# Optimization experiments

Measured on AMD Instinct MI355X. Metric: run time of the kernel, lower is better.

## Reference

```python
import jax, jax.numpy as jnp
import numpy as np
from jax import lax

V_PATCH_NUMS = (1, 2, 4, 8, 16)
BETA = 0.25
QUANT_RESI = 0.5
NUM_PHI = 4  # share_quant_resi=4 -> PhiPartiallyShared

# PhiPartiallyShared tick lookup (K=4 -> linspace(1/12, 11/12, 4))
def _phi_indices():
    K = NUM_PHI
    ticks = np.linspace(1/3/K, 1 - 1/3/K, K) if K == 4 else np.linspace(1/2/K, 1 - 1/2/K, K)
    SN = len(V_PATCH_NUMS)
    return [int(np.argmin(np.abs(ticks - si/(SN-1)))) for si in range(SN)]

PHI_IDX = _phi_indices()  # [0, 1, 1, 2, 3]


def phi_apply(h, w, b, ratio=QUANT_RESI):
    # h_out = (1-a)*h + a*Conv3x3(h), padding=1
    conv = lax.conv_general_dilated(h, w, (1, 1), 'SAME',
                                    dimension_numbers=('NCHW', 'OIHW', 'NCHW'))
    conv = conv + b[None, :, None, None]
    return h * (1.0 - ratio) + conv * ratio


def vq_forward(f_BChw, emb_w, phi_w, phi_b):
    f = f_BChw.astype(jnp.float32)
    B, C, H, W = f.shape
    f_ng = lax.stop_gradient(f)
    f_rest = f_ng
    f_hat = jnp.zeros_like(f)
    SN = len(V_PATCH_NUMS)
    loss = jnp.float32(0.0)
    emb_ng = lax.stop_gradient(emb_w)  # distances use .data (no grad)
    e_sq = jnp.sum(emb_ng * emb_ng, axis=1)  # [V]
    for si, pn in enumerate(V_PATCH_NUMS):
        if si != SN - 1:
            k = H // pn  # exact area pooling (divisible sizes)
            z = f_rest.reshape(B, C, pn, k, pn, k).mean(axis=(3, 5))
        else:
            z = f_rest
        z_NC = z.transpose(0, 2, 3, 1).reshape(-1, C)  # [B*pn*pn, C]
        # squared L2 distance to every code, argmin
        d = (jnp.sum(z_NC * z_NC, axis=1, keepdims=True) + e_sq
             - 2.0 * z_NC @ emb_ng.T)  # [N, V]
        idx = jnp.argmin(d, axis=1)  # [N]
        h = emb_w[idx].reshape(B, pn, pn, C).transpose(0, 3, 1, 2)  # [B,C,pn,pn]
        if si != SN - 1:
            h = jax.image.resize(h, (B, C, H, W), method='cubic')  # bicubic upsample
        pi = PHI_IDX[si]
        h = phi_apply(h, phi_w[pi], phi_b[pi])
        f_hat = f_hat + h
        f_rest = f_rest - h
        loss = loss + (BETA * jnp.mean((lax.stop_gradient(f_hat) - f) ** 2)
                       + jnp.mean((f_hat - f_ng) ** 2))
    loss = loss / SN
    # straight-through estimator
    f_hat_out = lax.stop_gradient(f_hat) - f_ng + f
    return f_hat_out, loss


def setup_inputs() -> dict:
    key = jax.random.key(0)
    k1, k2, k3 = jax.random.split(key, 3)
    B, C, H, W = 64, 32, 16, 16
    V = 4096
    f_BChw = jax.random.normal(k1, (B, C, H, W), dtype=jnp.float32)
    emb_w = jax.random.normal(k2, (V, C), dtype=jnp.float32) * 0.5
    phi_w = jax.random.normal(k3, (NUM_PHI, C, C, 3, 3), dtype=jnp.float32) * 0.05
    phi_b = jnp.zeros((NUM_PHI, C), dtype=jnp.float32)
    return {'f_BChw': f_BChw, 'emb_w': emb_w, 'phi_w': phi_w, 'phi_b': phi_b}


def reference(f_BChw, emb_w, phi_w, phi_b):
    return vq_forward(f_BChw, emb_w, phi_w, phi_b)
```

## Files before the change

### kernel.cpp

```cpp
#include <hip/hip_runtime.h>

typedef unsigned long long u64;

#define B_ 64
#define C_ 32
#define H_ 16
#define W_ 16
#define V_ 4096
#define NELEM_ (B_*C_*H_*W_)
#define NPOS_TOTAL 21824


__device__ __forceinline__ float keys_cubic(float x) {
  if (x >= 2.f) return 0.f;
  if (x >= 1.f) return ((-0.5f*x + 2.5f)*x - 4.f)*x + 2.f;
  return (1.5f*x - 2.5f)*x*x + 1.f;
}

__device__ __forceinline__ u64 pack_key(float d, int idx) {
  unsigned bu = __float_as_uint(d);
  unsigned m = bu ^ ((bu >> 31) ? 0xFFFFFFFFu : 0x80000000u);
  return ((u64)m << 32) | (unsigned)idx;
}


__global__ void init_kernel(const float* __restrict__ f, const float* __restrict__ emb,
                            float* __restrict__ f_rest, float* __restrict__ f_hat,
                            float* __restrict__ e_sq, u64* __restrict__ part,
                            float* __restrict__ loss_part) {
  int i = blockIdx.x*blockDim.x + threadIdx.x;
  if (i < NELEM_) { f_rest[i] = f[i]; f_hat[i] = 0.f; }
  if (i < NPOS_TOTAL) part[i] = ~0ull;
  if (i < 5*256) loss_part[i] = 0.f;
  if (i < V_) {
    const float4* p = (const float4*)(emb + (size_t)i*32);
    float s = 0.f;
#pragma unroll
    for (int j = 0; j < 8; ++j) { float4 q = p[j]; s += q.x*q.x + q.y*q.y + q.z*q.z + q.w*q.w; }
    e_sq[i] = s;
  }
}


__global__ void pool_kernel(const float* __restrict__ f_rest, float* __restrict__ z,
                            int pn, int k) {
  int t = blockIdx.x*blockDim.x + threadIdx.x;
  int N = B_*pn*pn;
  if (t >= N*C_) return;
  int n = t >> 5, c = t & 31;
  int pn2 = pn*pn;
  int b = n / pn2, rem = n % pn2;
  int y = rem / pn, x = rem % pn;
  const float* base = f_rest + (((size_t)b*C_ + c)*H_ + y*k)*W_ + x*k;
  float s = 0.f;
  if (k >= 4) {
    const float4* b4 = (const float4*)base;
    for (int ky = 0; ky < k; ++ky)
      for (int kx = 0; kx < (k>>2); ++kx) {
        float4 q = b4[ky*4 + kx];
        s += (q.x + q.y) + (q.z + q.w);
      }
  } else if (k == 2) {
    const float2* b2 = (const float2*)base;
    s = (b2[0].x + b2[0].y) + (b2[8].x + b2[8].y);
  } else {
    s = base[0];
  }
  z[(size_t)n*32 + c] = s * (1.f/(float)(k*k));
}


template<int P, int TILE>
__global__ void __launch_bounds__(256) argmin2_kernel(
    const float* __restrict__ z, const float* __restrict__ emb,
    const float* __restrict__ e_sq, u64* __restrict__ part, int cpc) {
  __shared__ float cl[TILE*32];
  __shared__ float es[TILE];
  const int tid = threadIdx.x;
  const int n0 = blockIdx.x*256*P + tid;
  float zb[P][32]; float zz[P];
#pragma unroll
  for (int p = 0; p < P; ++p) {
    const float4* zp = (const float4*)(z + (size_t)(n0 + p*256)*32);
#pragma unroll
    for (int i = 0; i < 8; ++i) {
      float4 q = zp[i];
      zb[p][4*i+0]=q.x; zb[p][4*i+1]=q.y; zb[p][4*i+2]=q.z; zb[p][4*i+3]=q.w;
    }
    float s = 0.f;
#pragma unroll
    for (int i = 0; i < 32; ++i) s = fmaf(zb[p][i], zb[p][i], s);
    zz[p] = s;
  }
  const int v0 = blockIdx.y * cpc;
  float bd[P]; int bi[P];
#pragma unroll
  for (int p = 0; p < P; ++p) { bd[p] = 3.4e38f; bi[p] = 0; }
  for (int t0 = 0; t0 < cpc; t0 += TILE) {
    __syncthreads();
    const float4* src = (const float4*)(emb + (size_t)(v0 + t0)*32);
    for (int e = tid; e < TILE*8; e += 256) ((float4*)cl)[e] = src[e];
    if (tid < TILE) es[tid] = e_sq[v0 + t0 + tid];
    __syncthreads();
    for (int c = 0; c < TILE; ++c) {
      const float4* cp = (const float4*)(cl + c*32);
      float4 q[8];
#pragma unroll
      for (int i = 0; i < 8; ++i) q[i] = cp[i];
      float ev = es[c];
#pragma unroll
      for (int p = 0; p < P; ++p) {
        float a0=0.f, a1=0.f, a2=0.f, a3=0.f;
#pragma unroll
        for (int i = 0; i < 8; ++i) {
          a0 = fmaf(zb[p][4*i+0], q[i].x, a0);
          a1 = fmaf(zb[p][4*i+1], q[i].y, a1);
          a2 = fmaf(zb[p][4*i+2], q[i].z, a2);
          a3 = fmaf(zb[p][4*i+3], q[i].w, a3);
        }
        float dot = (a0+a1)+(a2+a3);
        float d = (zz[p] + ev) - 2.f*dot;
        bool lt = d < bd[p];
        bd[p] = lt ? d : bd[p];
        bi[p] = lt ? (v0 + t0 + c) : bi[p];
      }
    }
  }
#pragma unroll
  for (int p = 0; p < P; ++p)
    atomicMin(part + n0 + p*256, pack_key(bd[p], bi[p]));
}

__global__ void __launch_bounds__(256) argmin0_kernel(
    const float* __restrict__ z, const float* __restrict__ emb,
    const float* __restrict__ e_sq, u64* __restrict__ part) {
  __shared__ float cl[64*32];
  __shared__ float es[64];
  const int tid = threadIdx.x;
  const int v0 = blockIdx.x * 64;
  const float4* src = (const float4*)(emb + (size_t)v0*32);
  for (int e = tid; e < 64*8; e += 256) ((float4*)cl)[e] = src[e];
  if (tid < 64) es[tid] = e_sq[v0 + tid];
  __syncthreads();
  const int p = tid & 63, sub = tid >> 6;
  float zb[32];
  const float4* zp = (const float4*)(z + (size_t)p*32);
#pragma unroll
  for (int i = 0; i < 8; ++i) {
    float4 q = zp[i];
    zb[4*i+0]=q.x; zb[4*i+1]=q.y; zb[4*i+2]=q.z; zb[4*i+3]=q.w;
  }
  float zz = 0.f;
#pragma unroll
  for (int i = 0; i < 32; ++i) zz = fmaf(zb[i], zb[i], zz);
  float bd = 3.4e38f; int bi = 0;
  for (int c = sub*16; c < sub*16 + 16; ++c) {
    const float4* cp = (const float4*)(cl + c*32);
    float4 q[8];
#pragma unroll
    for (int i = 0; i < 8; ++i) q[i] = cp[i];
    float a0=0.f, a1=0.f, a2=0.f, a3=0.f;
#pragma unroll
    for (int i = 0; i < 8; ++i) {
      a0 = fmaf(zb[4*i+0], q[i].x, a0);
      a1 = fmaf(zb[4*i+1], q[i].y, a1);
      a2 = fmaf(zb[4*i+2], q[i].z, a2);
      a3 = fmaf(zb[4*i+3], q[i].w, a3);
    }
    float dot = (a0+a1)+(a2+a3);
    float d = (zz + es[c]) - 2.f*dot;
    if (d < bd) { bd = d; bi = v0 + c; }
  }
  atomicMin(part + p, pack_key(bd, bi));
}


template<int PN>
__global__ void __launch_bounds__(512) upconv_kernel(
    const u64* __restrict__ part_s,
    const float* __restrict__ emb,
    const float* __restrict__ phi_w,
    const float* __restrict__ phi_b,
    const float* __restrict__ f,
    float* __restrict__ f_hat,
    float* __restrict__ f_rest,
    float* __restrict__ loss_part)
{
  constexpr int PN2 = PN*PN;
  const int b = blockIdx.x;
  const int cg = blockIdx.y;
  const int tid = threadIdx.x;

  __shared__ int   idx_s[PN2];
  __shared__ float W4[16][4];
  __shared__ int   I0[16];
  __shared__ float tmp_s[(PN < 16) ? C_*PN*16 : 1];
  union HupHs { float hup[C_*16*18]; float hs[C_*16*18]; };
  __shared__ HupHs u;
  __shared__ float wsum[8];

  for (int p = tid; p < PN2; p += 512)
    idx_s[p] = (int)(part_s[b*PN2 + p] & 0xFFFFFFFFull);

  if (PN < 16 && tid < 16) {
    float sf = (tid + 0.5f) * ((float)PN/16.f) - 0.5f;
    int i0 = (int)floorf(sf) - 1;
    float w[4]; float tot = 0.f;
#pragma unroll
    for (int t = 0; t < 4; ++t) {
      int i = i0 + t;
      float wv = (i >= 0 && i < PN) ? keys_cubic(fabsf(sf - (float)i)) : 0.f;
      w[t] = wv; tot += wv;
    }
    float r = 1.f/tot;
#pragma unroll
    for (int t = 0; t < 4; ++t) W4[tid][t] = w[t]*r;
    I0[tid] = i0;
  }
  __syncthreads();

  if (PN < 16) {
    for (int e = tid; e < C_*PN2; e += 512) {
      int c = e / PN2, p = e % PN2;
      u.hs[c*PN2 + p] = emb[(size_t)idx_s[p]*32 + c];
    }
  } else {
    for (int e = tid; e < C_*256; e += 512) {
      int c = e >> 8, p = e & 255;
      int y = p >> 4, x = p & 15;
      u.hup[(c*16 + y)*18 + 1 + x] = emb[(size_t)idx_s[p]*32 + c];
    }
    for (int e = tid; e < C_*16; e += 512) { u.hup[e*18] = 0.f; u.hup[e*18 + 17] = 0.f; }
  }
  __syncthreads();

  if (PN < 16) {
    for (int e = tid; e < C_*PN*16; e += 512) {
      int jx = e & 15; int rest = e >> 4;
      int iy = rest % PN; int c = rest / PN;
      int i0 = I0[jx];
      float s = 0.f;
#pragma unroll
      for (int t = 0; t < 4; ++t) {
        int ix = i0 + t; int ixc = min(max(ix, 0), PN-1);
        s += W4[jx][t] * u.hs[(c*PN + iy)*PN + ixc];
      }
      tmp_s[(c*PN + iy)*16 + jx] = s;
    }
    __syncthreads();
    for (int e = tid; e < C_*16; e += 512) { u.hup[e*18] = 0.f; u.hup[e*18 + 17] = 0.f; }
    for (int e = tid; e < C_*256; e += 512) {
      int jx = e & 15; int jy = (e >> 4) & 15; int c = e >> 8;
      int i0 = I0[jy];
      float s = 0.f;
#pragma unroll
      for (int t = 0; t < 4; ++t) {
        int iy = i0 + t; int iyc = min(max(iy, 0), PN-1);
        s += W4[jy][t] * tmp_s[(c*PN + iyc)*16 + jx];
      }
      u.hup[(c*16 + jy)*18 + 1 + jx] = s;
    }
    __syncthreads();
  }

  const int px = tid & 255;
  const int g  = tid >> 8;
  const int y  = px >> 4, x = px & 15;
  const int co0 = cg*8 + g*4;
  const float* wbase = phi_w + (size_t)co0*32*9;
  float acc[4];
#pragma unroll
  for (int o = 0; o < 4; ++o) acc[o] = phi_b[co0 + o];
  for (int ci = 0; ci < 32; ++ci) {
    float wn[9];
#pragma unroll
    for (int ky = 0; ky < 3; ++ky) {
      int yy = y + ky - 1;
      bool v = (yy >= 0 && yy <= 15);
      const float* r = &u.hup[(ci*16 + (v ? yy : 0))*18 + x];
      wn[ky*3+0] = v ? r[0] : 0.f;
      wn[ky*3+1] = v ? r[1] : 0.f;
      wn[ky*3+2] = v ? r[2] : 0.f;
    }
#pragma unroll
    for (int o = 0; o < 4; ++o) {
      const float* wp = wbase + ((size_t)o*32 + ci)*9;
#pragma unroll
      for (int t = 0; t < 9; ++t) acc[o] = fmaf(wp[t], wn[t], acc[o]);
    }
  }
  float lsum = 0.f;
#pragma unroll
  for (int o = 0; o < 4; ++o) {
    int co = co0 + o;
    float hv = 0.5f*u.hup[(co*16 + y)*18 + 1 + x] + 0.5f*acc[o];
    size_t gi = (((size_t)b*C_ + co)*16 + y)*16 + x;
    float fh = f_hat[gi] + hv;
    f_hat[gi] = fh;
    f_rest[gi] -= hv;
    float dd = fh - f[gi];
    lsum = fmaf(dd, dd, lsum);
  }
#pragma unroll
  for (int off = 32; off > 0; off >>= 1) lsum += __shfl_down(lsum, off);
  if ((tid & 63) == 0) wsum[tid >> 6] = lsum;
  __syncthreads();
  if (tid == 0) {
    float s = 0.f;
#pragma unroll
    for (int i = 0; i < 8; ++i) s += wsum[i];
    loss_part[blockIdx.y*64 + blockIdx.x] = s;
  }
}

__global__ void loss_kernel(const float* __restrict__ loss_part, float* __restrict__ out_loss) {
  __shared__ float s[256];
  int t = threadIdx.x;
  float v = 0.f;
#pragma unroll
  for (int i = 0; i < 5; ++i) v += loss_part[i*256 + t];
  s[t] = v;
  __syncthreads();
  for (int off = 128; off > 0; off >>= 1) {
    if (t < off) s[t] += s[t + off];
    __syncthreads();
  }
  if (t == 0) out_loss[0] = s[0] * (1.25f / (5.f * (float)NELEM_));
}


extern "C" void kernel_launch(void* const* d_in, const int* in_sizes, int n_in,
                              void* d_out, int out_size, void* d_ws, size_t ws_size,
                              hipStream_t stream) {
  const float* f     = (const float*)d_in[0];
  const float* emb   = (const float*)d_in[1];
  const float* phi_w = (const float*)d_in[2];
  const float* phi_b = (const float*)d_in[3];
  float* f_hat    = (float*)d_out;
  float* out_loss = f_hat + NELEM_;

  char* ws = (char*)d_ws;
  float* f_rest = (float*)ws;
  float* z      = f_rest + NELEM_;
  u64*   part   = (u64*)(z + NELEM_);
  float* e_sq   = (float*)(part + NPOS_TOTAL);
  float* loss_part = e_sq + V_;

  init_kernel<<<NELEM_/256, 256, 0, stream>>>(f, emb, f_rest, f_hat, e_sq, part, loss_part);

  const int PNs[5]   = {1,2,4,8,16};
  const int PHI[5]   = {0,1,2,2,3};
  const int PBASE[5] = {0, 64, 320, 1344, 5440};

  for (int si = 0; si < 5; ++si) {
    int pn = PNs[si], k = 16/pn, N = B_*pn*pn;
    pool_kernel<<<(N*C_ + 255)/256, 256, 0, stream>>>(f_rest, z, pn, k);
    u64* ps = part + PBASE[si];
    switch (si) {
      case 0: argmin0_kernel<<<64, 256, 0, stream>>>(z, emb, e_sq, ps); break;
      case 1: argmin2_kernel<1,16><<<dim3(1,256), 256, 0, stream>>>(z, emb, e_sq, ps, 16); break;
      case 2: argmin2_kernel<1,64><<<dim3(4,64),  256, 0, stream>>>(z, emb, e_sq, ps, 64); break;
      case 3: argmin2_kernel<2,64><<<dim3(8,64),  256, 0, stream>>>(z, emb, e_sq, ps, 64); break;
      case 4: argmin2_kernel<2,64><<<dim3(32,32), 256, 0, stream>>>(z, emb, e_sq, ps, 128); break;
    }
    const float* pw = phi_w + (size_t)PHI[si]*32*32*9;
    const float* pb = phi_b + (size_t)PHI[si]*32;
    dim3 cgrid(B_, 4);
    float* lp = loss_part + si*256;
    switch (pn) {
      case 1:  upconv_kernel<1 ><<<cgrid,512,0,stream>>>(ps, emb, pw, pb, f, f_hat, f_rest, lp); break;
      case 2:  upconv_kernel<2 ><<<cgrid,512,0,stream>>>(ps, emb, pw, pb, f, f_hat, f_rest, lp); break;
      case 4:  upconv_kernel<4 ><<<cgrid,512,0,stream>>>(ps, emb, pw, pb, f, f_hat, f_rest, lp); break;
      case 8:  upconv_kernel<8 ><<<cgrid,512,0,stream>>>(ps, emb, pw, pb, f, f_hat, f_rest, lp); break;
      case 16: upconv_kernel<16><<<cgrid,512,0,stream>>>(ps, emb, pw, pb, f, f_hat, f_rest, lp); break;
    }
  }
  loss_kernel<<<1, 256, 0, stream>>>(loss_part, out_loss);
}
```

Measured before the change: 270.8 us.

## Fuse pooling into upconv epilogue, drop init pass, retune argmin tiling

Removes the separate pool kernels by having each upconv kernel write the next scale's pooled residual (or the full residual layout) directly from shared memory. The init kernel no longer copies f into f_rest or zeroes f_hat; the first upconv handles that through a FIRST template flag, and scale-0 pooling moves into a small setup kernel. Argmin launch shapes and per-thread position counts are retuned, with launch_bounds occupancy hints and partial unrolling added. This cuts kernel launches and global round-trips at the cost of more shared memory and an extra sync in upconv.

```diff
diff --git a/kernel.cpp b/kernel.cpp
--- a/kernel.cpp
+++ b/kernel.cpp
@@ -24,14 +24,11 @@
 }
 
 
-__global__ void init_kernel(const float* __restrict__ f, const float* __restrict__ emb,
-                            float* __restrict__ f_rest, float* __restrict__ f_hat,
-                            float* __restrict__ e_sq, u64* __restrict__ part,
-                            float* __restrict__ loss_part) {
+__global__ void setup_kernel(const float* __restrict__ f, const float* __restrict__ emb,
+                             float* __restrict__ e_sq, u64* __restrict__ part,
+                             float* __restrict__ z0) {
   int i = blockIdx.x*blockDim.x + threadIdx.x;
-  if (i < NELEM_) { f_rest[i] = f[i]; f_hat[i] = 0.f; }
   if (i < NPOS_TOTAL) part[i] = ~0ull;
-  if (i < 5*256) loss_part[i] = 0.f;
   if (i < V_) {
     const float4* p = (const float4*)(emb + (size_t)i*32);
     float s = 0.f;
@@ -39,45 +36,23 @@
     for (int j = 0; j < 8; ++j) { float4 q = p[j]; s += q.x*q.x + q.y*q.y + q.z*q.z + q.w*q.w; }
     e_sq[i] = s;
   }
-}
-
-
-__global__ void pool_kernel(const float* __restrict__ f_rest, float* __restrict__ z,
-                            int pn, int k) {
-  int t = blockIdx.x*blockDim.x + threadIdx.x;
-  int N = B_*pn*pn;
-  if (t >= N*C_) return;
-  int n = t >> 5, c = t & 31;
-  int pn2 = pn*pn;
-  int b = n / pn2, rem = n % pn2;
-  int y = rem / pn, x = rem % pn;
-  const float* base = f_rest + (((size_t)b*C_ + c)*H_ + y*k)*W_ + x*k;
-  float s = 0.f;
-  if (k >= 4) {
-    const float4* b4 = (const float4*)base;
-    for (int ky = 0; ky < k; ++ky)
-      for (int kx = 0; kx < (k>>2); ++kx) {
-        float4 q = b4[ky*4 + kx];
-        s += (q.x + q.y) + (q.z + q.w);
-      }
-  } else if (k == 2) {
-    const float2* b2 = (const float2*)base;
-    s = (b2[0].x + b2[0].y) + (b2[8].x + b2[8].y);
-  } else {
-    s = base[0];
-  }
-  z[(size_t)n*32 + c] = s * (1.f/(float)(k*k));
+  if (i < B_*C_) {
+    const float4* p = (const float4*)(f + (size_t)i*256);
+    float s = 0.f;
+    for (int j = 0; j < 64; ++j) { float4 q = p[j]; s += (q.x + q.y) + (q.z + q.w); }
+    z0[i] = s * (1.f/256.f);
+  }
 }
 
 
 template<int P, int TILE>
-__global__ void __launch_bounds__(256) argmin2_kernel(
+__global__ void __launch_bounds__(256, 2) argmin2_kernel(
     const float* __restrict__ z, const float* __restrict__ emb,
     const float* __restrict__ e_sq, u64* __restrict__ part, int cpc) {
   __shared__ float cl[TILE*32];
   __shared__ float es[TILE];
   const int tid = threadIdx.x;
-  const int n0 = blockIdx.x*256*P + tid;
+  const int n0 = blockIdx.x*(256*P) + tid;
   float zb[P][32]; float zz[P];
 #pragma unroll
   for (int p = 0; p < P; ++p) {
@@ -95,13 +70,14 @@
   const int v0 = blockIdx.y * cpc;
   float bd[P]; int bi[P];
 #pragma unroll
-  for (int p = 0; p < P; ++p) { bd[p] = 3.4e38f; bi[p] = 0; }
+  for (int p = 0; p < P; ++p) { bd[p] = 3.4e38f; bi[p] = v0; }
   for (int t0 = 0; t0 < cpc; t0 += TILE) {
     __syncthreads();
     const float4* src = (const float4*)(emb + (size_t)(v0 + t0)*32);
     for (int e = tid; e < TILE*8; e += 256) ((float4*)cl)[e] = src[e];
     if (tid < TILE) es[tid] = e_sq[v0 + t0 + tid];
     __syncthreads();
+#pragma unroll 2
     for (int c = 0; c < TILE; ++c) {
       const float4* cp = (const float4*)(cl + c*32);
       float4 q[8];
@@ -153,7 +129,7 @@
   float zz = 0.f;
 #pragma unroll
   for (int i = 0; i < 32; ++i) zz = fmaf(zb[i], zb[i], zz);
-  float bd = 3.4e38f; int bi = 0;
+  float bd = 3.4e38f; int bi = v0;
   for (int c = sub*16; c < sub*16 + 16; ++c) {
     const float4* cp = (const float4*)(cl + c*32);
     float4 q[8];
@@ -175,7 +151,7 @@
 }
 
 
-template<int PN>
+template<int PN, int NEXT_PN, bool FIRST>
 __global__ void __launch_bounds__(512) upconv_kernel(
     const u64* __restrict__ part_s,
     const float* __restrict__ emb,
@@ -184,9 +160,11 @@
     const float* __restrict__ f,
     float* __restrict__ f_hat,
     float* __restrict__ f_rest,
+    float* __restrict__ z_next,
     float* __restrict__ loss_part)
 {
   constexpr int PN2 = PN*PN;
+  constexpr bool POOLED = (NEXT_PN != 0 && NEXT_PN < 16);
   const int b = blockIdx.x;
   const int cg = blockIdx.y;
   const int tid = threadIdx.x;
@@ -195,6 +173,7 @@
   __shared__ float W4[16][4];
   __shared__ int   I0[16];
   __shared__ float tmp_s[(PN < 16) ? C_*PN*16 : 1];
+  __shared__ float pool_s[POOLED ? 8*256 : 1];
   union HupHs { float hup[C_*16*18]; float hs[C_*16*18]; };
   __shared__ HupHs u;
   __shared__ float wsum[8];
@@ -289,17 +268,42 @@
       for (int t = 0; t < 9; ++t) acc[o] = fmaf(wp[t], wn[t], acc[o]);
     }
   }
+
   float lsum = 0.f;
 #pragma unroll
   for (int o = 0; o < 4; ++o) {
     int co = co0 + o;
     float hv = 0.5f*u.hup[(co*16 + y)*18 + 1 + x] + 0.5f*acc[o];
     size_t gi = (((size_t)b*C_ + co)*16 + y)*16 + x;
-    float fh = f_hat[gi] + hv;
+    float fv = f[gi];
+    float fh = FIRST ? hv : (f_hat[gi] + hv);
     f_hat[gi] = fh;
-    f_rest[gi] -= hv;
-    float dd = fh - f[gi];
+    if constexpr (NEXT_PN != 0) {
+      float nfr = FIRST ? (fv - hv) : (f_rest[gi] - hv);
+      f_rest[gi] = nfr;
+      if constexpr (NEXT_PN == 16) {
+        z_next[((size_t)b*256 + px)*32 + co] = nfr;
+      } else {
+        pool_s[(g*4 + o)*256 + px] = nfr;
+      }
+    }
+    float dd = fh - fv;
     lsum = fmaf(dd, dd, lsum);
+  }
+  if constexpr (POOLED) {
+    constexpr int NP = (NEXT_PN > 0) ? NEXT_PN : 1;
+    constexpr int NP2 = NP*NP;
+    constexpr int KP = 16/NP;
+    __syncthreads();
+    if (tid < 8*NP2) {
+      int c_l = tid / NP2, p = tid % NP2;
+      int yy = (p / NP)*KP, xx = (p % NP)*KP;
+      float s = 0.f;
+      for (int a = 0; a < KP; ++a)
+        for (int e = 0; e < KP; ++e)
+          s += pool_s[c_l*256 + (yy + a)*16 + xx + e];
+      z_next[((size_t)b*NP2 + p)*32 + cg*8 + c_l] = s * (1.f/(float)(KP*KP));
+    }
   }
 #pragma unroll
   for (int off = 32; off > 0; off >>= 1) lsum += __shfl_down(lsum, off);
@@ -346,34 +350,29 @@
   float* e_sq   = (float*)(part + NPOS_TOTAL);
   float* loss_part = e_sq + V_;
 
-  init_kernel<<<NELEM_/256, 256, 0, stream>>>(f, emb, f_rest, f_hat, e_sq, part, loss_part);
-
-  const int PNs[5]   = {1,2,4,8,16};
-  const int PHI[5]   = {0,1,2,2,3};
-  const int PBASE[5] = {0, 64, 320, 1344, 5440};
-
-  for (int si = 0; si < 5; ++si) {
-    int pn = PNs[si], k = 16/pn, N = B_*pn*pn;
-    pool_kernel<<<(N*C_ + 255)/256, 256, 0, stream>>>(f_rest, z, pn, k);
-    u64* ps = part + PBASE[si];
-    switch (si) {
-      case 0: argmin0_kernel<<<64, 256, 0, stream>>>(z, emb, e_sq, ps); break;
-      case 1: argmin2_kernel<1,16><<<dim3(1,256), 256, 0, stream>>>(z, emb, e_sq, ps, 16); break;
-      case 2: argmin2_kernel<1,64><<<dim3(4,64),  256, 0, stream>>>(z, emb, e_sq, ps, 64); break;
-      case 3: argmin2_kernel<2,64><<<dim3(8,64),  256, 0, stream>>>(z, emb, e_sq, ps, 64); break;
-      case 4: argmin2_kernel<2,64><<<dim3(32,32), 256, 0, stream>>>(z, emb, e_sq, ps, 128); break;
-    }
-    const float* pw = phi_w + (size_t)PHI[si]*32*32*9;
-    const float* pb = phi_b + (size_t)PHI[si]*32;
-    dim3 cgrid(B_, 4);
-    float* lp = loss_part + si*256;
-    switch (pn) {
-      case 1:  upconv_kernel<1 ><<<cgrid,512,0,stream>>>(ps, emb, pw, pb, f, f_hat, f_rest, lp); break;
-      case 2:  upconv_kernel<2 ><<<cgrid,512,0,stream>>>(ps, emb, pw, pb, f, f_hat, f_rest, lp); break;
-      case 4:  upconv_kernel<4 ><<<cgrid,512,0,stream>>>(ps, emb, pw, pb, f, f_hat, f_rest, lp); break;
-      case 8:  upconv_kernel<8 ><<<cgrid,512,0,stream>>>(ps, emb, pw, pb, f, f_hat, f_rest, lp); break;
-      case 16: upconv_kernel<16><<<cgrid,512,0,stream>>>(ps, emb, pw, pb, f, f_hat, f_rest, lp); break;
-    }
-  }
+  const float* pw0 = phi_w;                 const float* pb0 = phi_b;
+  const float* pw1 = phi_w + 1*32*32*9;     const float* pb1 = phi_b + 1*32;
+  const float* pw2 = phi_w + 2*32*32*9;     const float* pb2 = phi_b + 2*32;
+  const float* pw3 = phi_w + 3*32*32*9;     const float* pb3 = phi_b + 3*32;
+
+  setup_kernel<<<(NPOS_TOTAL + 255)/256, 256, 0, stream>>>(f, emb, e_sq, part, z);
+
+  dim3 cgrid(B_, 4);
+  argmin0_kernel<<<64, 256, 0, stream>>>(z, emb, e_sq, part + 0);
+  upconv_kernel<1, 2, true><<<cgrid, 512, 0, stream>>>(part + 0, emb, pw0, pb0,
+      f, f_hat, f_rest, z, loss_part + 0*256);
+  argmin2_kernel<1,16><<<dim3(1,256), 256, 0, stream>>>(z, emb, e_sq, part + 64, 16);
+  upconv_kernel<2, 4, false><<<cgrid, 512, 0, stream>>>(part + 64, emb, pw1, pb1,
+      f, f_hat, f_rest, z, loss_part + 1*256);
+  argmin2_kernel<2,32><<<dim3(2,128), 256, 0, stream>>>(z, emb, e_sq, part + 320, 32);
+  upconv_kernel<4, 8, false><<<cgrid, 512, 0, stream>>>(part + 320, emb, pw2, pb2,
+      f, f_hat, f_rest, z, loss_part + 2*256);
+  argmin2_kernel<4,64><<<dim3(4,64), 256, 0, stream>>>(z, emb, e_sq, part + 1344, 64);
+  upconv_kernel<8, 16, false><<<cgrid, 512, 0, stream>>>(part + 1344, emb, pw2, pb2,
+      f, f_hat, f_rest, z, loss_part + 3*256);
+  argmin2_kernel<4,64><<<dim3(16,32), 256, 0, stream>>>(z, emb, e_sq, part + 5440, 128);
+  upconv_kernel<16, 0, false><<<cgrid, 512, 0, stream>>>(part + 5440, emb, pw3, pb3,
+      f, f_hat, f_rest, z, loss_part + 4*256);
+
   loss_kernel<<<1, 256, 0, stream>>>(loss_part, out_loss);
 }
```

Result: faster. 240.2 us (-11.3%).
